# Performance work log

Measured on AMD Instinct MI355X. Metric: run time of the kernel, lower is better.

## Reference

```python
import jax, jax.numpy as jnp
import numpy as np
import math

EMB = 512

def setup_inputs() -> dict:
    key = jax.random.key(0)
    ks = jax.random.split(key, 7)
    B, L, E = 4, 4096, EMB
    s = 1.0 / math.sqrt(E)
    return {
        "x": jax.random.normal(ks[0], (B, L, E), dtype=jnp.float32),
        "Wq": jax.random.normal(ks[1], (E, E), dtype=jnp.float32) * s,
        "bq": jax.random.normal(ks[2], (E,), dtype=jnp.float32) * 0.01,
        "Wk": jax.random.normal(ks[3], (E, E), dtype=jnp.float32) * s,
        "bk": jax.random.normal(ks[4], (E,), dtype=jnp.float32) * 0.01,
        "Wv": jax.random.normal(ks[5], (E, E), dtype=jnp.float32) * s,
        "bv": jax.random.normal(ks[6], (E,), dtype=jnp.float32) * 0.01,
    }

def reference(x, Wq, bq, Wk, bk, Wv, bv):
    # x: [B, L, E]; Linear weights stored torch-style [out, in]
    E = x.shape[-1]
    L = x.shape[1]
    q = jnp.einsum('ble,fe->blf', x, Wq) + bq
    k = jnp.einsum('ble,fe->blf', x, Wk) + bk
    v = jnp.einsum('ble,fe->blf', x, Wv) + bv
    qk = jnp.einsum('bqe,bke->bqk', q, k)  # [B, L, L]
    # causal mask: strict upper triangle filled with -1e9 BEFORE scaling (as in source)
    mask = jnp.triu(jnp.ones((L, L), dtype=bool), k=1)
    qk = jnp.where(mask, jnp.float32(-1e9), qk)
    att = jax.nn.softmax(qk / jnp.sqrt(jnp.float32(E)), axis=-1)
    return jnp.einsum('bqk,bke->bqe', att, v)
```

## Files before the change

### kernel.cpp

```cpp
#include <hip/hip_runtime.h>

typedef unsigned short u16;
typedef unsigned int u32;
typedef short bf16x8 __attribute__((ext_vector_type(8)));
typedef float f32x4 __attribute__((ext_vector_type(4)));
typedef u16 u16x8 __attribute__((ext_vector_type(8)));
typedef u16 u16x4 __attribute__((ext_vector_type(4)));

typedef const __attribute__((address_space(1))) u32* gas_ptr;
typedef __attribute__((address_space(3))) u32* las_ptr;

#define LQ   4096
#define EMB  512
#define NB   4
#define MROWS (NB * LQ)
#define QSCALE 0.04419417382415922f

__device__ __forceinline__ u16 f2bf(float f) {
  unsigned u = __builtin_bit_cast(unsigned, f);
  u += 0x7fffu + ((u >> 16) & 1u);
  return (u16)(u >> 16);
}
__device__ __forceinline__ float bf2f(u16 h) {
  unsigned u = ((unsigned)h) << 16;
  return __builtin_bit_cast(float, u);
}

__global__ void prep_w(const float* __restrict__ Wq, const float* __restrict__ bq,
                       const float* __restrict__ Wk, const float* __restrict__ bk,
                       const float* __restrict__ Wv, const float* __restrict__ bv,
                       u16* __restrict__ wqb, u16* __restrict__ wkb, u16* __restrict__ wvb,
                       float* __restrict__ bias) {
  int i = blockIdx.x * 256 + threadIdx.x;
  if (i < EMB * EMB) {
    wqb[i] = f2bf(Wq[i] * QSCALE);
    wkb[i] = f2bf(Wk[i]);
    wvb[i] = f2bf(Wv[i]);
  }
  if (i < EMB) {
    bias[i]           = bq[i] * QSCALE;
    bias[EMB + i]     = bk[i];
    bias[2 * EMB + i] = bv[i];
  }
}

__global__ void prep_x(const float* __restrict__ x, u16* __restrict__ xb) {
  int i = blockIdx.x * 256 + threadIdx.x;
  const float4* p = (const float4*)(x + (size_t)i * 8);
  float4 a = p[0], b = p[1];
  u16x8 o;
  o[0] = f2bf(a.x); o[1] = f2bf(a.y); o[2] = f2bf(a.z); o[3] = f2bf(a.w);
  o[4] = f2bf(b.x); o[5] = f2bf(b.y); o[6] = f2bf(b.z); o[7] = f2bf(b.w);
  *(u16x8*)(xb + (size_t)i * 8) = o;
}

__device__ __forceinline__ void stage128_256t(const u16* g, int ld, u16* lds, int tid) {
  int wave = tid >> 6;
#pragma unroll
  for (int p = 0; p < 4; ++p) {
    int c = tid + p * 256;
    int row = c >> 3, hh = c & 7;
    int h = hh ^ (row & 7);
    const u16* src = g + (size_t)row * ld + h * 8;
    u16* dst = lds + wave * 512 + p * 2048;
    __builtin_amdgcn_global_load_lds((gas_ptr)(const void*)src, (las_ptr)(void*)dst, 16, 0, 0);
  }
}

__device__ __forceinline__ void gemm_core_db(
    const u16* __restrict__ A, int lda,
    const u16* __restrict__ B, int ldb,
    int kIters, u16* lds,
    f32x4 acc[4][4], int tid, int lane, int wr, int wc)
{
  stage128_256t(A, lda, lds, tid);
  stage128_256t(B, ldb, lds + 8192, tid);
  for (int kb = 0; kb < kIters; ++kb) {
    u16* ldsA = lds + (kb & 1) * 16384;
    u16* ldsB = ldsA + 8192;
    __syncthreads();
    if (kb + 1 < kIters) {
      u16* nA = lds + ((kb + 1) & 1) * 16384;
      stage128_256t(A + (kb + 1) * 64, lda, nA, tid);
      stage128_256t(B + (kb + 1) * 64, ldb, nA + 8192, tid);
    }
#pragma unroll
    for (int s = 0; s < 2; ++s) {
      bf16x8 af[4], bfr[4];
#pragma unroll
      for (int m = 0; m < 4; ++m) {
        int row = wr * 64 + m * 16 + (lane & 15);
        int hh = (s * 4 + (lane >> 4)) ^ (row & 7);
        af[m] = *(const bf16x8*)(ldsA + row * 64 + hh * 8);
      }
#pragma unroll
      for (int n = 0; n < 4; ++n) {
        int row = wc * 64 + n * 16 + (lane & 15);
        int hh = (s * 4 + (lane >> 4)) ^ (row & 7);
        bfr[n] = *(const bf16x8*)(ldsB + row * 64 + hh * 8);
      }
#pragma unroll
      for (int m = 0; m < 4; ++m)
#pragma unroll
        for (int n = 0; n < 4; ++n)
          acc[m][n] = __builtin_amdgcn_mfma_f32_16x16x32_bf16(af[m], bfr[n], acc[m][n], 0, 0, 0);
    }
  }
}

__global__ __launch_bounds__(256, 2) void k_qkv(
    const u16* __restrict__ xb,
    const u16* __restrict__ w0, const u16* __restrict__ w1, const u16* __restrict__ w2,
    const float* __restrict__ bias,
    u16* __restrict__ o0, u16* __restrict__ o1, u16* __restrict__ o2)
{
  __shared__ __align__(16) u16 lds[32768];
  int bi = blockIdx.x;
  int which = bi >> 9;
  int t = bi & 511;
  int rt = t >> 2, ct = t & 3;
  const u16* W = (which == 0) ? w0 : (which == 1) ? w1 : w2;
  const float* bs = bias + which * EMB;
  int tid = threadIdx.x, lane = tid & 63, wave = tid >> 6;
  int wr = wave >> 1, wc = wave & 1;
  f32x4 acc[4][4];
#pragma unroll
  for (int m = 0; m < 4; ++m)
#pragma unroll
    for (int n = 0; n < 4; ++n) acc[m][n] = (f32x4)0.0f;

  gemm_core_db(xb + (size_t)rt * 128 * EMB, EMB,
               W + (size_t)ct * 128 * EMB, EMB, EMB / 64,
               lds, acc, tid, lane, wr, wc);

#pragma unroll
  for (int m = 0; m < 4; ++m)
#pragma unroll
    for (int n = 0; n < 4; ++n) {
      int row0 = rt * 128 + wr * 64 + m * 16 + ((lane >> 4) << 2);
      int col  = ct * 128 + wc * 64 + n * 16 + (lane & 15);
      float bv = bs[col];
      if (which < 2) {
        u16* out = (which == 0) ? o0 : o1;
#pragma unroll
        for (int r = 0; r < 4; ++r)
          out[(size_t)(row0 + r) * EMB + col] = f2bf(acc[m][n][r] + bv);
      } else {
        int b = row0 >> 12, l0 = row0 & (LQ - 1);
        u16x4 pk;
#pragma unroll
        for (int r = 0; r < 4; ++r) pk[r] = f2bf(acc[m][n][r] + bv);
        *(u16x4*)(o2 + ((size_t)(b * EMB + col)) * LQ + l0) = pk;
      }
    }
}

__global__ __launch_bounds__(256, 2) void k_qk(
    const u16* __restrict__ Q, const u16* __restrict__ K,
    u16* __restrict__ S, int bstart)
{
  __shared__ __align__(16) u16 lds[32768];
  int t = blockIdx.x;
  int b_local = t / 528;
  int i = t - b_local * 528;
  int qi = (int)((sqrtf(8.f * (float)i + 1.f) - 1.f) * 0.5f);
  while ((qi + 1) * (qi + 2) / 2 <= i) ++qi;
  while (qi * (qi + 1) / 2 > i) --qi;
  int ki = i - qi * (qi + 1) / 2;
  int bg = bstart + b_local;

  int tid = threadIdx.x, lane = tid & 63, wave = tid >> 6;
  int wr = wave >> 1, wc = wave & 1;
  f32x4 acc[4][4];
#pragma unroll
  for (int m = 0; m < 4; ++m)
#pragma unroll
    for (int n = 0; n < 4; ++n) acc[m][n] = (f32x4)0.0f;

  gemm_core_db(Q + ((size_t)bg * LQ + qi * 128) * EMB, EMB,
               K + ((size_t)bg * LQ + ki * 128) * EMB, EMB, EMB / 64,
               lds, acc, tid, lane, wr, wc);

  u16* Sb = S + (size_t)b_local * LQ * LQ;
#pragma unroll
  for (int m = 0; m < 4; ++m)
#pragma unroll
    for (int n = 0; n < 4; ++n) {
      int row0 = qi * 128 + wr * 64 + m * 16 + ((lane >> 4) << 2);
      int col  = ki * 128 + wc * 64 + n * 16 + (lane & 15);
#pragma unroll
      for (int r = 0; r < 4; ++r) {
        int row = row0 + r;
        float v = (col > row) ? -1e9f : acc[m][n][r];
        Sb[(size_t)row * LQ + col] = f2bf(v);
      }
    }
}

__global__ __launch_bounds__(512, 1) void k_pv2(
    const u16* __restrict__ S, const u16* __restrict__ Vt,
    float* __restrict__ out, int bstart, int bcount)
{
  __shared__ __align__(16) u16 lds[32768];
  int bi = blockIdx.x;
  int per = 4 * bcount;
  int pairidx = bi / per;
  int rem = bi - pairidx * per;
  int ct = rem / bcount;
  int b_local = rem - ct * bcount;
  int bg = bstart + b_local;

  int rtA = pairidx, rtB = 31 - pairidx;
  int unitsA = 2 * (rtA + 1);
  int total = unitsA + 2 * (rtB + 1);

  const u16* Sbase = S + (size_t)b_local * LQ * LQ;
  const u16* Bp = Vt + ((size_t)bg * EMB + ct * 128) * LQ;

  int tid = threadIdx.x, lane = tid & 63, wave = tid >> 6;
  int wr = wave >> 2, wc = wave & 3;
  wr = wave >> 1; wc = wave & 1;
  int l15 = lane & 15, lhi = lane >> 4;

  f32x4 acc[2][4];
#pragma unroll
  for (int m = 0; m < 2; ++m)
#pragma unroll
    for (int n = 0; n < 4; ++n) acc[m][n] = (f32x4)0.0f;
  float mrun[2] = {-3.0e38f, -3.0e38f};
  float lrun[2] = {0.f, 0.f};

  auto stage_unit = [&](int i) {
    int ph = (i >= unitsA);
    int kb = ph ? (i - unitsA) : i;
    int rt = ph ? rtB : rtA;
    const u16* ga = Sbase + ((size_t)rt * 128) * LQ + kb * 64;
    const u16* gb = Bp + kb * 64;
    u16* buf = lds + (i & 1) * 16384;
#pragma unroll
    for (int p = 0; p < 2; ++p) {
      int c = tid + p * 512;
      int row = c >> 3, hh = c & 7;
      int h = hh ^ (row & 7);
      __builtin_amdgcn_global_load_lds((gas_ptr)(const void*)(ga + (size_t)row * LQ + h * 8),
                                       (las_ptr)(void*)(buf + wave * 512 + p * 4096), 16, 0, 0);
      __builtin_amdgcn_global_load_lds((gas_ptr)(const void*)(gb + (size_t)row * LQ + h * 8),
                                       (las_ptr)(void*)(buf + 8192 + wave * 512 + p * 4096), 16, 0, 0);
    }
  };

  auto epilogue = [&](int rt) {
#pragma unroll
    for (int m = 0; m < 2; ++m) {
      float linv = 1.0f / lrun[m];
#pragma unroll
      for (int r = 0; r < 4; ++r) {
        float fr = __shfl(linv, lhi * 4 + r);
        int grow = rt * 128 + wr * 32 + m * 16 + lhi * 4 + r;
#pragma unroll
        for (int n = 0; n < 4; ++n) {
          int col = ct * 128 + wc * 64 + n * 16 + l15;
          out[((size_t)bg * LQ + grow) * EMB + col] = acc[m][n][r] * fr;
        }
      }
    }
#pragma unroll
    for (int m = 0; m < 2; ++m) {
#pragma unroll
      for (int n = 0; n < 4; ++n) acc[m][n] = (f32x4)0.0f;
      mrun[m] = -3.0e38f;
      lrun[m] = 0.f;
    }
  };

  stage_unit(0);

  for (int i = 0; i < total; ++i) {
    u16* ldsA = lds + (i & 1) * 16384;
    u16* ldsB = ldsA + 8192;
    __syncthreads();
    if (i + 1 < total) stage_unit(i + 1);
    if (i == unitsA) epilogue(rtA);

    float sv[2][16];
#pragma unroll
    for (int m = 0; m < 2; ++m) {
      int row = wr * 32 + m * 16 + l15;
#pragma unroll
      for (int s = 0; s < 2; ++s) {
        int hh = (s * 4 + lhi) ^ (row & 7);
        u16x8 raw = *(const u16x8*)(ldsA + row * 64 + hh * 8);
#pragma unroll
        for (int j = 0; j < 8; ++j) sv[m][s * 8 + j] = bf2f(raw[j]);
      }
    }
    float tmax[2];
#pragma unroll
    for (int m = 0; m < 2; ++m) {
      float tm = sv[m][0];
#pragma unroll
      for (int k = 1; k < 16; ++k) tm = fmaxf(tm, sv[m][k]);
      tm = fmaxf(tm, __shfl_xor(tm, 16));
      tm = fmaxf(tm, __shfl_xor(tm, 32));
      tmax[m] = tm;
    }
    bool need = (tmax[0] > mrun[0] + 8.f) || (tmax[1] > mrun[1] + 8.f);
    if (__any(need)) {
#pragma unroll
      for (int m = 0; m < 2; ++m) {
        float mn = fmaxf(mrun[m], tmax[m]);
        float f = __expf(mrun[m] - mn);
        mrun[m] = mn;
        lrun[m] *= f;
#pragma unroll
        for (int r = 0; r < 4; ++r) {
          float fr = __shfl(f, lhi * 4 + r);
#pragma unroll
          for (int n = 0; n < 4; ++n) acc[m][n][r] *= fr;
        }
      }
    }
    u16x8 pf[2][2];
#pragma unroll
    for (int m = 0; m < 2; ++m) {
      float ts = 0.f;
#pragma unroll
      for (int s = 0; s < 2; ++s)
#pragma unroll
        for (int j = 0; j < 8; ++j) {
          float p = __expf(sv[m][s * 8 + j] - mrun[m]);
          ts += p;
          pf[m][s][j] = f2bf(p);
        }
      ts += __shfl_xor(ts, 16);
      ts += __shfl_xor(ts, 32);
      lrun[m] += ts;
    }
#pragma unroll
    for (int s = 0; s < 2; ++s) {
#pragma unroll
      for (int n = 0; n < 4; ++n) {
        int col = wc * 64 + n * 16 + l15;
        int hh = (s * 4 + lhi) ^ (col & 7);
        bf16x8 bv = *(const bf16x8*)(ldsB + col * 64 + hh * 8);
#pragma unroll
        for (int m = 0; m < 2; ++m)
          acc[m][n] = __builtin_amdgcn_mfma_f32_16x16x32_bf16(
              __builtin_bit_cast(bf16x8, pf[m][s]), bv, acc[m][n], 0, 0, 0);
      }
    }
  }
  epilogue(rtB);
}

extern "C" void kernel_launch(void* const* d_in, const int* in_sizes, int n_in,
                              void* d_out, int out_size, void* d_ws, size_t ws_size,
                              hipStream_t stream) {
  const float* x  = (const float*)d_in[0];
  const float* Wq = (const float*)d_in[1];
  const float* bq = (const float*)d_in[2];
  const float* Wk = (const float*)d_in[3];
  const float* bk = (const float*)d_in[4];
  const float* Wv = (const float*)d_in[5];
  const float* bv = (const float*)d_in[6];

  char* ws = (char*)d_ws;
  size_t off = 0;
  u16* xb  = (u16*)(ws + off); off += (size_t)MROWS * EMB * 2;
  u16* wqb = (u16*)(ws + off); off += (size_t)EMB * EMB * 2;
  u16* wkb = (u16*)(ws + off); off += (size_t)EMB * EMB * 2;
  u16* wvb = (u16*)(ws + off); off += (size_t)EMB * EMB * 2;
  float* bias = (float*)(ws + off); off += 3 * EMB * 4;
  off = (off + 255) & ~(size_t)255;
  u16* Qb  = (u16*)(ws + off); off += (size_t)MROWS * EMB * 2;
  u16* Kb  = (u16*)(ws + off); off += (size_t)MROWS * EMB * 2;
  u16* Vtb = (u16*)(ws + off); off += (size_t)MROWS * EMB * 2;
  size_t fixed = off;
  size_t s_full = (size_t)NB * LQ * LQ * 2;
  int bcap = (ws_size >= fixed + s_full) ? NB : 1;
  u16* Sb = (u16*)(ws + fixed);

  prep_w<<<(EMB * EMB + 255) / 256, 256, 0, stream>>>(Wq, bq, Wk, bk, Wv, bv,
                                                      wqb, wkb, wvb, bias);
  prep_x<<<(MROWS * EMB / 8) / 256, 256, 0, stream>>>(x, xb);

  k_qkv<<<1536, 256, 0, stream>>>(xb, wqb, wkb, wvb, bias, Qb, Kb, Vtb);

  for (int bs = 0; bs < NB; bs += bcap) {
    int bc = (bs + bcap <= NB) ? bcap : (NB - bs);
    k_qk<<<528 * bc, 256, 0, stream>>>(Qb, Kb, Sb, bs);
    k_pv2<<<64 * bc, 512, 0, stream>>>(Sb, Vtb, (float*)d_out, bs, bc);
  }
}
```

Baseline: 244.7 us.

## Restructure PV kernel so each block covers all output columns for 32 rows

```diff
diff --git a/kernel.cpp b/kernel.cpp
--- a/kernel.cpp
+++ b/kernel.cpp
@@ -201,155 +201,150 @@
     const u16* __restrict__ S, const u16* __restrict__ Vt,
     float* __restrict__ out, int bstart, int bcount)
 {
-  __shared__ __align__(16) u16 lds[32768];
+  __shared__ __align__(16) u16 sA[4096];
+  __shared__ __align__(16) u16 sB[65536];
+  __shared__ __align__(16) u16 sP[2048];
+  __shared__ float sF[32];
+  __shared__ float sL[32];
+
   int bi = blockIdx.x;
-  int per = 4 * bcount;
-  int pairidx = bi / per;
-  int rem = bi - pairidx * per;
-  int ct = rem / bcount;
-  int b_local = rem - ct * bcount;
+  int pairidx = bi / bcount;
+  int b_local = bi - pairidx * bcount;
   int bg = bstart + b_local;
-
-  int rtA = pairidx, rtB = 31 - pairidx;
-  int unitsA = 2 * (rtA + 1);
-  int total = unitsA + 2 * (rtB + 1);
+  int rtA = pairidx, rtB = 127 - pairidx;
+  int unitsA = (rtA + 2) >> 1;
+  int total = unitsA + ((rtB + 2) >> 1);
 
   const u16* Sbase = S + (size_t)b_local * LQ * LQ;
-  const u16* Bp = Vt + ((size_t)bg * EMB + ct * 128) * LQ;
+  const u16* Vb = Vt + (size_t)bg * EMB * LQ;
 
   int tid = threadIdx.x, lane = tid & 63, wave = tid >> 6;
-  int wr = wave >> 2, wc = wave & 3;
-  wr = wave >> 1; wc = wave & 1;
   int l15 = lane & 15, lhi = lane >> 4;
+  int srow = tid >> 4;
+  int scg  = tid & 15;
+  int shh  = ((scg >> 1) ^ (srow & 7)) * 8 + (scg & 1) * 4;
 
   f32x4 acc[2][4];
 #pragma unroll
   for (int m = 0; m < 2; ++m)
 #pragma unroll
     for (int n = 0; n < 4; ++n) acc[m][n] = (f32x4)0.0f;
-  float mrun[2] = {-3.0e38f, -3.0e38f};
-  float lrun[2] = {0.f, 0.f};
+  float mrun = -3.0e38f, lrun = 0.f;
 
   auto stage_unit = [&](int i) {
-    int ph = (i >= unitsA);
-    int kb = ph ? (i - unitsA) : i;
+    int ph = (i >= unitsA) ? 1 : 0;
     int rt = ph ? rtB : rtA;
-    const u16* ga = Sbase + ((size_t)rt * 128) * LQ + kb * 64;
-    const u16* gb = Bp + kb * 64;
-    u16* buf = lds + (i & 1) * 16384;
-#pragma unroll
-    for (int p = 0; p < 2; ++p) {
-      int c = tid + p * 512;
-      int row = c >> 3, hh = c & 7;
-      int h = hh ^ (row & 7);
-      __builtin_amdgcn_global_load_lds((gas_ptr)(const void*)(ga + (size_t)row * LQ + h * 8),
-                                       (las_ptr)(void*)(buf + wave * 512 + p * 4096), 16, 0, 0);
-      __builtin_amdgcn_global_load_lds((gas_ptr)(const void*)(gb + (size_t)row * LQ + h * 8),
-                                       (las_ptr)(void*)(buf + 8192 + wave * 512 + p * 4096), 16, 0, 0);
+    int k0 = (ph ? (i - unitsA) : i) * 64;
+    const u16* ga = Sbase + (size_t)(rt * 32) * LQ + k0;
+    const u16* gb = Vb + k0;
+    u16* bA = sA + (i & 1) * 2048;
+    u16* bB = sB + (i & 1) * 32768;
+    if (wave < 4) {
+      int ca = wave * 64 + lane;
+      int row = ca >> 3, h = ca & 7;
+      __builtin_amdgcn_global_load_lds(
+          (gas_ptr)(const void*)(ga + (size_t)row * LQ + (h ^ (row & 7)) * 8),
+          (las_ptr)(void*)(bA + wave * 512), 16, 0, 0);
+    }
+#pragma unroll
+    for (int p = 0; p < 8; ++p) {
+      int cb = wave * 512 + p * 64 + lane;
+      int col = cb >> 3, h = cb & 7;
+      __builtin_amdgcn_global_load_lds(
+          (gas_ptr)(const void*)(gb + (size_t)col * LQ + (h ^ (col & 7)) * 8),
+          (las_ptr)(void*)(bB + wave * 4096 + p * 512), 16, 0, 0);
     }
   };
 
   auto epilogue = [&](int rt) {
-#pragma unroll
-    for (int m = 0; m < 2; ++m) {
-      float linv = 1.0f / lrun[m];
+    if (scg == 0) sL[srow] = 1.0f / lrun;
+    __syncthreads();
+    float li[2][4];
+#pragma unroll
+    for (int m = 0; m < 2; ++m)
+#pragma unroll
+      for (int r = 0; r < 4; ++r) li[m][r] = sL[m * 16 + lhi * 4 + r];
+#pragma unroll
+    for (int m = 0; m < 2; ++m)
 #pragma unroll
       for (int r = 0; r < 4; ++r) {
-        float fr = __shfl(linv, lhi * 4 + r);
-        int grow = rt * 128 + wr * 32 + m * 16 + lhi * 4 + r;
+        int grow = rt * 32 + m * 16 + lhi * 4 + r;
 #pragma unroll
         for (int n = 0; n < 4; ++n) {
-          int col = ct * 128 + wc * 64 + n * 16 + l15;
-          out[((size_t)bg * LQ + grow) * EMB + col] = acc[m][n][r] * fr;
+          int col = wave * 64 + n * 16 + l15;
+          out[((size_t)bg * LQ + grow) * EMB + col] = acc[m][n][r] * li[m][r];
         }
       }
-    }
-#pragma unroll
-    for (int m = 0; m < 2; ++m) {
+#pragma unroll
+    for (int m = 0; m < 2; ++m)
 #pragma unroll
       for (int n = 0; n < 4; ++n) acc[m][n] = (f32x4)0.0f;
-      mrun[m] = -3.0e38f;
-      lrun[m] = 0.f;
-    }
+    mrun = -3.0e38f;
+    lrun = 0.f;
   };
 
   stage_unit(0);
 
   for (int i = 0; i < total; ++i) {
-    u16* ldsA = lds + (i & 1) * 16384;
-    u16* ldsB = ldsA + 8192;
+    u16* bA = sA + (i & 1) * 2048;
+    u16* bB = sB + (i & 1) * 32768;
     __syncthreads();
     if (i + 1 < total) stage_unit(i + 1);
     if (i == unitsA) epilogue(rtA);
 
-    float sv[2][16];
-#pragma unroll
-    for (int m = 0; m < 2; ++m) {
-      int row = wr * 32 + m * 16 + l15;
-#pragma unroll
-      for (int s = 0; s < 2; ++s) {
+    u16x4 raw = *(const u16x4*)(bA + srow * 64 + shh);
+    float s0 = bf2f(raw[0]), s1 = bf2f(raw[1]), s2 = bf2f(raw[2]), s3 = bf2f(raw[3]);
+    float tmax = fmaxf(fmaxf(s0, s1), fmaxf(s2, s3));
+#pragma unroll
+    for (int off = 1; off <= 8; off <<= 1) tmax = fmaxf(tmax, __shfl_xor(tmax, off));
+    float mnew = (tmax > mrun + 8.f) ? tmax : mrun;
+    float f = __expf(mrun - mnew);
+    mrun = mnew;
+    float e0 = __expf(s0 - mrun), e1 = __expf(s1 - mrun);
+    float e2 = __expf(s2 - mrun), e3 = __expf(s3 - mrun);
+    float rs = (e0 + e1) + (e2 + e3);
+#pragma unroll
+    for (int off = 1; off <= 8; off <<= 1) rs += __shfl_xor(rs, off);
+    lrun = lrun * f + rs;
+    u16x4 pk;
+    pk[0] = f2bf(e0); pk[1] = f2bf(e1); pk[2] = f2bf(e2); pk[3] = f2bf(e3);
+    *(u16x4*)(sP + srow * 64 + shh) = pk;
+    if (scg == 0) sF[srow] = f;
+    __syncthreads();
+
+    float fr[2][4];
+#pragma unroll
+    for (int m = 0; m < 2; ++m)
+#pragma unroll
+      for (int r = 0; r < 4; ++r) fr[m][r] = sF[m * 16 + lhi * 4 + r];
+#pragma unroll
+    for (int m = 0; m < 2; ++m)
+#pragma unroll
+      for (int n = 0; n < 4; ++n)
+#pragma unroll
+        for (int r = 0; r < 4; ++r) acc[m][n][r] *= fr[m][r];
+
+#pragma unroll
+    for (int s = 0; s < 2; ++s) {
+      bf16x8 af[2];
+#pragma unroll
+      for (int m = 0; m < 2; ++m) {
+        int row = m * 16 + l15;
         int hh = (s * 4 + lhi) ^ (row & 7);
-        u16x8 raw = *(const u16x8*)(ldsA + row * 64 + hh * 8);
-#pragma unroll
-        for (int j = 0; j < 8; ++j) sv[m][s * 8 + j] = bf2f(raw[j]);
-      }
-    }
-    float tmax[2];
-#pragma unroll
-    for (int m = 0; m < 2; ++m) {
-      float tm = sv[m][0];
-#pragma unroll
-      for (int k = 1; k < 16; ++k) tm = fmaxf(tm, sv[m][k]);
-      tm = fmaxf(tm, __shfl_xor(tm, 16));
-      tm = fmaxf(tm, __shfl_xor(tm, 32));
-      tmax[m] = tm;
-    }
-    bool need = (tmax[0] > mrun[0] + 8.f) || (tmax[1] > mrun[1] + 8.f);
-    if (__any(need)) {
-#pragma unroll
-      for (int m = 0; m < 2; ++m) {
-        float mn = fmaxf(mrun[m], tmax[m]);
-        float f = __expf(mrun[m] - mn);
-        mrun[m] = mn;
-        lrun[m] *= f;
-#pragma unroll
-        for (int r = 0; r < 4; ++r) {
-          float fr = __shfl(f, lhi * 4 + r);
-#pragma unroll
-          for (int n = 0; n < 4; ++n) acc[m][n][r] *= fr;
-        }
-      }
-    }
-    u16x8 pf[2][2];
-#pragma unroll
-    for (int m = 0; m < 2; ++m) {
-      float ts = 0.f;
-#pragma unroll
-      for (int s = 0; s < 2; ++s)
-#pragma unroll
-        for (int j = 0; j < 8; ++j) {
-          float p = __expf(sv[m][s * 8 + j] - mrun[m]);
-          ts += p;
-          pf[m][s][j] = f2bf(p);
-        }
-      ts += __shfl_xor(ts, 16);
-      ts += __shfl_xor(ts, 32);
-      lrun[m] += ts;
-    }
-#pragma unroll
-    for (int s = 0; s < 2; ++s) {
+        af[m] = *(const bf16x8*)(sP + row * 64 + hh * 8);
+      }
 #pragma unroll
       for (int n = 0; n < 4; ++n) {
-        int col = wc * 64 + n * 16 + l15;
+        int col = wave * 64 + n * 16 + l15;
         int hh = (s * 4 + lhi) ^ (col & 7);
-        bf16x8 bv = *(const bf16x8*)(ldsB + col * 64 + hh * 8);
+        bf16x8 bv = *(const bf16x8*)(bB + col * 64 + hh * 8);
 #pragma unroll
         for (int m = 0; m < 2; ++m)
-          acc[m][n] = __builtin_amdgcn_mfma_f32_16x16x32_bf16(
-              __builtin_bit_cast(bf16x8, pf[m][s]), bv, acc[m][n], 0, 0, 0);
-      }
-    }
-  }
+          acc[m][n] = __builtin_amdgcn_mfma_f32_16x16x32_bf16(af[m], bv, acc[m][n], 0, 0, 0);
+      }
+    }
+  }
+  __syncthreads();
   epilogue(rtB);
 }
 
```

Result: no change. 244.4 us (-0.1%).
